# Kernel optimization log

Measured on AMD Instinct MI355X. Metric: run time of the kernel, lower is better.

## Reference

```python
import jax, jax.numpy as jnp
import numpy as np
from jax import lax

B, T, D, R, V = 128, 8, 2048, 4, 512

def setup_inputs() -> dict:
    key = jax.random.key(0)
    k0, k1, k2, k3, k4 = jax.random.split(key, 5)
    # scales chosen so the TT products stay within fp32 range (see notes)
    input_embs = jax.random.normal(k0, (B, T, D), dtype=jnp.float32) * 0.1
    label_ids = jax.random.randint(k1, (B, T), 0, V)
    w_alpha = jax.random.normal(k2, (D, R), dtype=jnp.float32) * 0.04
    w_beta = jax.random.normal(k3, (D, R), dtype=jnp.float32) * 0.04
    w_vocab = jax.random.normal(k4, (D, V * R * R), dtype=jnp.float32) * 0.04
    return {"input_embs": input_embs, "label_ids": label_ids,
            "w_alpha": w_alpha, "w_beta": w_beta, "w_vocab": w_vocab}

def _tt_loss(input_embs, w_alpha, w_beta, w_vocab, label_ids):
    b, t, d = input_embs.shape
    flat = input_embs.reshape(-1, d)                    # [B*T, D]
    alpha = jnp.abs((flat @ w_alpha).reshape(b, t, R).mean(1))   # [B, R]
    beta = jnp.abs((flat @ w_beta).reshape(b, t, R).mean(1))     # [B, R]
    core = jnp.abs((flat @ w_vocab).reshape(b, t, R, V, R).mean(1))  # [B, R, V, R]

    # --- _select: gather per-position R x R cores and chain-multiply ---
    core_v = core.transpose(0, 2, 1, 3)                 # [B, V, R, R]
    sel = jnp.take_along_axis(core_v, label_ids[:, :, None, None], axis=1)  # [B, T, R, R]
    sel_t = jnp.swapaxes(sel, 0, 1)                     # [T, B, R, R]

    def chain(carry, m):
        return jnp.einsum('bik,bkj->bij', carry, m), None
    res, _ = lax.scan(chain, sel_t[0], sel_t[1:])       # [B, R, R]
    u = jnp.einsum('bi,bij,bj->b', alpha, res, beta)    # unnormalized probs [B]

    # --- normalization constant: marg^(T+1) contracted with alpha/beta ---
    marg = core.sum(2)                                  # [B, R, R]

    def pow_step(c, _):
        return jnp.einsum('bik,bkj->bij', c, marg), None
    zmat, _ = lax.scan(pow_step, marg, None, length=t)  # marg^(t+1)
    z = jnp.einsum('bi,bij,bj->b', alpha, zmat, beta)

    loss = -jnp.log(u / z)
    return loss.mean()

def reference(input_embs, label_ids, w_alpha, w_beta, w_vocab):
    return _tt_loss(input_embs, w_alpha, w_beta, w_vocab, label_ids)
```

## Files before the change

kernel.cpp:

```cpp
#include <hip/hip_runtime.h>
#include <math.h>

#define BB 128
#define TT 8
#define DD 2048
#define RR 4
#define VV 512

typedef __attribute__((ext_vector_type(8))) short short8;
typedef __attribute__((ext_vector_type(4))) float v4f;

__device__ __forceinline__ unsigned pack_bf16(float x, float y) {
    union { float f; unsigned u; } a, b;
    a.f = x; b.f = y;
    unsigned ua = a.u + 0x7fffu + ((a.u >> 16) & 1u);
    unsigned ub = b.u + 0x7fffu + ((b.u >> 16) & 1u);
    return (ua >> 16) | (ub & 0xffff0000u);
}

__global__ __launch_bounds__(256) void phaseA(const float* __restrict__ inp,
                                              const float* __restrict__ w_alpha,
                                              const float* __restrict__ w_beta,
                                              unsigned short* __restrict__ fmb,
                                              float* __restrict__ alphaA,
                                              float* __restrict__ betaA) {
    int bid = blockIdx.x;
    int b = bid >> 1, half = bid & 1;
    int tid = threadIdx.x;
    const float* base = inp + (size_t)b * TT * DD;
    float pa[4] = {0.f, 0.f, 0.f, 0.f};
    float pb[4] = {0.f, 0.f, 0.f, 0.f};
#pragma unroll
    for (int i = 0; i < 4; ++i) {
        int d = half * 1024 + i * 256 + tid;
        float s = 0.f;
#pragma unroll
        for (int t = 0; t < TT; ++t) s += base[t * DD + d];
        float v = s * (1.0f / TT);
        union { float f; unsigned u; } cv; cv.f = v;
        unsigned r = cv.u + 0x7fffu + ((cv.u >> 16) & 1u);
        fmb[b * DD + d] = (unsigned short)(r >> 16);
        float4 wa = *(const float4*)(w_alpha + d * 4);
        float4 wb = *(const float4*)(w_beta + d * 4);
        pa[0] += v * wa.x; pa[1] += v * wa.y; pa[2] += v * wa.z; pa[3] += v * wa.w;
        pb[0] += v * wb.x; pb[1] += v * wb.y; pb[2] += v * wb.z; pb[3] += v * wb.w;
    }
#pragma unroll
    for (int r = 0; r < 4; ++r) {
        for (int m = 1; m < 64; m <<= 1) {
            pa[r] += __shfl_xor(pa[r], m);
            pb[r] += __shfl_xor(pb[r], m);
        }
    }
    if ((tid & 63) == 0) {
#pragma unroll
        for (int r = 0; r < 4; ++r) {
            atomicAdd(&alphaA[b * 4 + r], pa[r]);
            atomicAdd(&betaA[b * 4 + r], pb[r]);
        }
    }
}

__global__ __launch_bounds__(512, 2) void phaseB(const unsigned short* __restrict__ fmb,
                                                 const float* __restrict__ wv,
                                                 const int* __restrict__ labels,
                                                 float* __restrict__ margA,
                                                 float* __restrict__ sel) {
    __shared__ unsigned short Ws[2][32][136];
    __shared__ int slab[BB * TT];

    const int tid = threadIdx.x;
    const int nb = blockIdx.x;
    const int col0 = nb * 32;

    slab[tid] = labels[tid];
    slab[tid + 512] = labels[tid + 512];

    const int nq = tid & 7;
    const int kp = tid >> 3;
    const int w = tid >> 6;
    const int lane = tid & 63;
    const int m15 = lane & 15;
    const int q = lane >> 4;

    const float* wbase = wv + (size_t)(2 * kp) * 8192 + col0 + nq * 4;
    const unsigned short* abase = fmb + (w * 16 + m15) * DD + q * 8;

    v4f acc0 = {0.f, 0.f, 0.f, 0.f};
    v4f acc1 = {0.f, 0.f, 0.f, 0.f};
    short8 afr[2][4];
    float4 sw0, sw1;

    sw0 = *(const float4*)(wbase);
    sw1 = *(const float4*)(wbase + 8192);
#pragma unroll
    for (int ks = 0; ks < 4; ++ks) afr[0][ks] = *(const short8*)(abase + ks * 32);
    {
        const float* f0 = (const float*)&sw0;
        const float* f1 = (const float*)&sw1;
#pragma unroll
        for (int j = 0; j < 4; ++j)
            *(unsigned*)&Ws[0][nq * 4 + j][2 * kp] = pack_bf16(f0[j], f1[j]);
    }
    __syncthreads();

    for (int c = 0; c < 16; ++c) {
        const int cur = c & 1;
        if (c < 15) {
            const float* wp = wbase + (size_t)(c + 1) * 128 * 8192;
            sw0 = *(const float4*)(wp);
            sw1 = *(const float4*)(wp + 8192);
            const unsigned short* ap = abase + (c + 1) * 128;
#pragma unroll
            for (int ks = 0; ks < 4; ++ks) afr[1 - cur][ks] = *(const short8*)(ap + ks * 32);
        }
#pragma unroll
        for (int ks = 0; ks < 4; ++ks) {
            short8 b0 = *(const short8*)&Ws[cur][m15][ks * 32 + q * 8];
            short8 b1 = *(const short8*)&Ws[cur][16 + m15][ks * 32 + q * 8];
            acc0 = __builtin_amdgcn_mfma_f32_16x16x32_bf16(afr[cur][ks], b0, acc0, 0, 0, 0);
            acc1 = __builtin_amdgcn_mfma_f32_16x16x32_bf16(afr[cur][ks], b1, acc1, 0, 0, 0);
        }
        if (c < 15) {
            const float* f0 = (const float*)&sw0;
            const float* f1 = (const float*)&sw1;
#pragma unroll
            for (int j = 0; j < 4; ++j)
                *(unsigned*)&Ws[1 - cur][nq * 4 + j][2 * kp] = pack_bf16(f0[j], f1[j]);
        }
        __syncthreads();
    }

    const int vbase = (nb & 63) * 8;
    const int iblk = nb >> 6;
    const int j = m15 & 3;
    const int v0 = vbase + (m15 >> 2);
    const float* a0p = (const float*)&acc0;
    const float* a1p = (const float*)&acc1;
#pragma unroll
    for (int r = 0; r < 4; ++r) {
        int m = w * 16 + q * 4 + r;
        float a0 = fabsf(a0p[r]);
        float a1 = fabsf(a1p[r]);
        float s = a0 + a1;
        s += __shfl_xor(s, 4);
        s += __shfl_xor(s, 8);
        if ((lane & 12) == 0) atomicAdd(&margA[m * 16 + iblk * 4 + j], s);
#pragma unroll
        for (int t = 0; t < TT; ++t) {
            int lv = slab[m * 8 + t];
            if (lv == v0)     sel[(m * 8 + t) * 16 + iblk * 4 + j] = a0;
            if (lv == v0 + 4) sel[(m * 8 + t) * 16 + iblk * 4 + j] = a1;
        }
    }
}

__global__ __launch_bounds__(128) void phaseD(const float* __restrict__ alpha,
                                              const float* __restrict__ beta,
                                              const float* __restrict__ marg,
                                              const float* __restrict__ sel,
                                              float* __restrict__ out) {
    int b = threadIdx.x;
    const float* sb = sel + b * TT * 16;
    float res[16], tmp[16], mm[16], zm[16];
#pragma unroll
    for (int e = 0; e < 16; ++e) res[e] = sb[e];
    for (int t = 1; t < TT; ++t) {
        const float* m = sb + t * 16;
#pragma unroll
        for (int i = 0; i < 4; ++i)
#pragma unroll
            for (int jj = 0; jj < 4; ++jj) {
                float s = 0.f;
#pragma unroll
                for (int k = 0; k < 4; ++k) s += res[i * 4 + k] * m[k * 4 + jj];
                tmp[i * 4 + jj] = s;
            }
#pragma unroll
        for (int e = 0; e < 16; ++e) res[e] = tmp[e];
    }
#pragma unroll
    for (int e = 0; e < 16; ++e) { mm[e] = marg[b * 16 + e]; zm[e] = mm[e]; }
    for (int st = 0; st < TT; ++st) {
#pragma unroll
        for (int i = 0; i < 4; ++i)
#pragma unroll
            for (int jj = 0; jj < 4; ++jj) {
                float s = 0.f;
#pragma unroll
                for (int k = 0; k < 4; ++k) s += zm[i * 4 + k] * mm[k * 4 + jj];
                tmp[i * 4 + jj] = s;
            }
#pragma unroll
        for (int e = 0; e < 16; ++e) zm[e] = tmp[e];
    }
    float u = 0.f, z = 0.f;
#pragma unroll
    for (int i = 0; i < 4; ++i) {
        float ai = fabsf(alpha[b * 4 + i]);
#pragma unroll
        for (int jj = 0; jj < 4; ++jj) {
            float bj = fabsf(beta[b * 4 + jj]);
            u += ai * res[i * 4 + jj] * bj;
            z += ai * zm[i * 4 + jj] * bj;
        }
    }
    float loss = logf(z) - logf(u);
    __shared__ float red[128];
    red[b] = loss;
    __syncthreads();
    for (int off = 64; off >= 1; off >>= 1) {
        if (b < off) red[b] += red[b + off];
        __syncthreads();
    }
    if (b == 0) out[0] = red[0] * (1.0f / BB);
}

extern "C" void kernel_launch(void* const* d_in, const int* in_sizes, int n_in,
                              void* d_out, int out_size, void* d_ws, size_t ws_size,
                              hipStream_t stream) {
    const float* inp     = (const float*)d_in[0];
    const int*   labels  = (const int*)d_in[1];
    const float* w_alpha = (const float*)d_in[2];
    const float* w_beta  = (const float*)d_in[3];
    const float* wv      = (const float*)d_in[4];
    float* out = (float*)d_out;

    float* ws    = (float*)d_ws;
    float* alpha = ws;
    float* beta  = ws + 512;
    float* marg  = ws + 1024;
    float* sel   = ws + 3072;
    unsigned short* fmb = (unsigned short*)(ws + 3072 + 16384);

    hipMemsetAsync(ws, 0, 3072 * sizeof(float), stream);

    phaseA<<<256, 256, 0, stream>>>(inp, w_alpha, w_beta, fmb, alpha, beta);
    phaseB<<<256, 512, 0, stream>>>(fmb, wv, labels, marg, sel);
    phaseD<<<1, 128, 0, stream>>>(alpha, beta, marg, sel, out);
}
```

Before: 129.4 us.

## Fuse final reduction into GEMM kernel via last-block counter and drop memset

Removes the hipMemsetAsync and the separate phaseD launch. phaseA now zeroes the marg buffer and the counter itself, and writes per-half alpha/beta partials without atomics. phaseBD has the last block to finish, found through an atomic counter with threadfences, compute the TT chains and the loss reduction. This cuts two launches from the stream at the cost of a global atomic and fences in every block.

```diff
diff --git a/kernel.cpp b/kernel.cpp
--- a/kernel.cpp
+++ b/kernel.cpp
@@ -22,11 +22,17 @@
                                               const float* __restrict__ w_alpha,
                                               const float* __restrict__ w_beta,
                                               unsigned short* __restrict__ fmb,
-                                              float* __restrict__ alphaA,
-                                              float* __restrict__ betaA) {
+                                              float* __restrict__ alphaP,
+                                              float* __restrict__ betaP,
+                                              float* __restrict__ marg,
+                                              unsigned* __restrict__ cnt) {
     int bid = blockIdx.x;
     int b = bid >> 1, half = bid & 1;
     int tid = threadIdx.x;
+
+    if (bid < 8) marg[bid * 256 + tid] = 0.f;
+    if (bid == 0 && tid == 0) *cnt = 0u;
+
     const float* base = inp + (size_t)b * TT * DD;
     float pa[4] = {0.f, 0.f, 0.f, 0.f};
     float pb[4] = {0.f, 0.f, 0.f, 0.f};
@@ -52,20 +58,28 @@
             pb[r] += __shfl_xor(pb[r], m);
         }
     }
+    __shared__ float sA[4][4], sB[4][4];
+    int wid = tid >> 6;
     if ((tid & 63) == 0) {
 #pragma unroll
-        for (int r = 0; r < 4; ++r) {
-            atomicAdd(&alphaA[b * 4 + r], pa[r]);
-            atomicAdd(&betaA[b * 4 + r], pb[r]);
-        }
-    }
-}
-
-__global__ __launch_bounds__(512, 2) void phaseB(const unsigned short* __restrict__ fmb,
-                                                 const float* __restrict__ wv,
-                                                 const int* __restrict__ labels,
-                                                 float* __restrict__ margA,
-                                                 float* __restrict__ sel) {
+        for (int r = 0; r < 4; ++r) { sA[wid][r] = pa[r]; sB[wid][r] = pb[r]; }
+    }
+    __syncthreads();
+    if (tid < 4) {
+        alphaP[b * 8 + half * 4 + tid] = sA[0][tid] + sA[1][tid] + sA[2][tid] + sA[3][tid];
+        betaP [b * 8 + half * 4 + tid] = sB[0][tid] + sB[1][tid] + sB[2][tid] + sB[3][tid];
+    }
+}
+
+__global__ __launch_bounds__(512, 2) void phaseBD(const unsigned short* __restrict__ fmb,
+                                                  const float* __restrict__ wv,
+                                                  const int* __restrict__ labels,
+                                                  float* __restrict__ margA,
+                                                  float* __restrict__ sel,
+                                                  const float* __restrict__ alphaP,
+                                                  const float* __restrict__ betaP,
+                                                  unsigned* __restrict__ cnt,
+                                                  float* __restrict__ out) {
     __shared__ unsigned short Ws[2][32][136];
     __shared__ int slab[BB * TT];
 
@@ -153,67 +167,72 @@
             if (lv == v0 + 4) sel[(m * 8 + t) * 16 + iblk * 4 + j] = a1;
         }
     }
-}
-
-__global__ __launch_bounds__(128) void phaseD(const float* __restrict__ alpha,
-                                              const float* __restrict__ beta,
-                                              const float* __restrict__ marg,
-                                              const float* __restrict__ sel,
-                                              float* __restrict__ out) {
-    int b = threadIdx.x;
-    const float* sb = sel + b * TT * 16;
-    float res[16], tmp[16], mm[16], zm[16];
-#pragma unroll
-    for (int e = 0; e < 16; ++e) res[e] = sb[e];
-    for (int t = 1; t < TT; ++t) {
-        const float* m = sb + t * 16;
-#pragma unroll
-        for (int i = 0; i < 4; ++i)
+
+    __threadfence();
+    __syncthreads();
+    __shared__ int amLast;
+    if (tid == 0) amLast = (atomicAdd(cnt, 1u) == 255u) ? 1 : 0;
+    __syncthreads();
+    if (!amLast) return;
+    __threadfence();
+
+    float loss = 0.f;
+    if (tid < 128) {
+        const int b = tid;
+        const float* sb = sel + b * TT * 16;
+        float res[16], tmp[16], mm[16], zm[16];
+#pragma unroll
+        for (int e = 0; e < 16; ++e) res[e] = sb[e];
+        for (int t = 1; t < TT; ++t) {
+            const float* m = sb + t * 16;
+#pragma unroll
+            for (int i = 0; i < 4; ++i)
+#pragma unroll
+                for (int jj = 0; jj < 4; ++jj) {
+                    float s = 0.f;
+#pragma unroll
+                    for (int k = 0; k < 4; ++k) s += res[i * 4 + k] * m[k * 4 + jj];
+                    tmp[i * 4 + jj] = s;
+                }
+#pragma unroll
+            for (int e = 0; e < 16; ++e) res[e] = tmp[e];
+        }
+#pragma unroll
+        for (int e = 0; e < 16; ++e) { mm[e] = margA[b * 16 + e]; zm[e] = mm[e]; }
+        for (int st = 0; st < TT; ++st) {
+#pragma unroll
+            for (int i = 0; i < 4; ++i)
+#pragma unroll
+                for (int jj = 0; jj < 4; ++jj) {
+                    float s = 0.f;
+#pragma unroll
+                    for (int k = 0; k < 4; ++k) s += zm[i * 4 + k] * mm[k * 4 + jj];
+                    tmp[i * 4 + jj] = s;
+                }
+#pragma unroll
+            for (int e = 0; e < 16; ++e) zm[e] = tmp[e];
+        }
+        float u = 0.f, z = 0.f;
+#pragma unroll
+        for (int i = 0; i < 4; ++i) {
+            float ai = fabsf(alphaP[b * 8 + i] + alphaP[b * 8 + 4 + i]);
 #pragma unroll
             for (int jj = 0; jj < 4; ++jj) {
-                float s = 0.f;
-#pragma unroll
-                for (int k = 0; k < 4; ++k) s += res[i * 4 + k] * m[k * 4 + jj];
-                tmp[i * 4 + jj] = s;
+                float bj = fabsf(betaP[b * 8 + jj] + betaP[b * 8 + 4 + jj]);
+                u += ai * res[i * 4 + jj] * bj;
+                z += ai * zm[i * 4 + jj] * bj;
             }
-#pragma unroll
-        for (int e = 0; e < 16; ++e) res[e] = tmp[e];
-    }
-#pragma unroll
-    for (int e = 0; e < 16; ++e) { mm[e] = marg[b * 16 + e]; zm[e] = mm[e]; }
-    for (int st = 0; st < TT; ++st) {
-#pragma unroll
-        for (int i = 0; i < 4; ++i)
-#pragma unroll
-            for (int jj = 0; jj < 4; ++jj) {
-                float s = 0.f;
-#pragma unroll
-                for (int k = 0; k < 4; ++k) s += zm[i * 4 + k] * mm[k * 4 + jj];
-                tmp[i * 4 + jj] = s;
-            }
-#pragma unroll
-        for (int e = 0; e < 16; ++e) zm[e] = tmp[e];
-    }
-    float u = 0.f, z = 0.f;
-#pragma unroll
-    for (int i = 0; i < 4; ++i) {
-        float ai = fabsf(alpha[b * 4 + i]);
-#pragma unroll
-        for (int jj = 0; jj < 4; ++jj) {
-            float bj = fabsf(beta[b * 4 + jj]);
-            u += ai * res[i * 4 + jj] * bj;
-            z += ai * zm[i * 4 + jj] * bj;
-        }
-    }
-    float loss = logf(z) - logf(u);
+        }
+        loss = logf(z) - logf(u);
+    }
     __shared__ float red[128];
-    red[b] = loss;
+    if (tid < 128) red[tid] = loss;
     __syncthreads();
     for (int off = 64; off >= 1; off >>= 1) {
-        if (b < off) red[b] += red[b + off];
+        if (tid < off) red[tid] += red[tid + off];
         __syncthreads();
     }
-    if (b == 0) out[0] = red[0] * (1.0f / BB);
+    if (tid == 0) out[0] = red[0] * (1.0f / BB);
 }
 
 extern "C" void kernel_launch(void* const* d_in, const int* in_sizes, int n_in,
@@ -226,16 +245,14 @@
     const float* wv      = (const float*)d_in[4];
     float* out = (float*)d_out;
 
-    float* ws    = (float*)d_ws;
-    float* alpha = ws;
-    float* beta  = ws + 512;
-    float* marg  = ws + 1024;
-    float* sel   = ws + 3072;
-    unsigned short* fmb = (unsigned short*)(ws + 3072 + 16384);
-
-    hipMemsetAsync(ws, 0, 3072 * sizeof(float), stream);
-
-    phaseA<<<256, 256, 0, stream>>>(inp, w_alpha, w_beta, fmb, alpha, beta);
-    phaseB<<<256, 512, 0, stream>>>(fmb, wv, labels, marg, sel);
-    phaseD<<<1, 128, 0, stream>>>(alpha, beta, marg, sel, out);
-}
+    float* ws     = (float*)d_ws;
+    float* alphaP = ws;
+    float* betaP  = ws + 1024;
+    float* marg   = ws + 2048;
+    float* sel    = ws + 4096;
+    unsigned* cnt = (unsigned*)(ws + 20480);
+    unsigned short* fmb = (unsigned short*)(ws + 20496);
+
+    phaseA<<<256, 256, 0, stream>>>(inp, w_alpha, w_beta, fmb, alphaP, betaP, marg, cnt);
+    phaseBD<<<256, 512, 0, stream>>>(fmb, wv, labels, marg, sel, alphaP, betaP, cnt, out);
+}
```

Result: slower. 153.7 us (+18.8%).
